# Performance work log

Hardware: AMD Instinct MI355X
Metric: run time of the kernel (lower is better)

The kernel has to match this reference:

```python
import jax, jax.numpy as jnp
import numpy as np

N_OBJ, N_SR, N_V, N_F = 8192, 4096, 4100, 4096
EPS = 1e-8


def setup_inputs() -> dict:
    key = jax.random.key(0)
    k1, k2, k3, k4, k5 = jax.random.split(key, 5)
    obj_points = jax.random.normal(k1, (N_OBJ, 3), jnp.float32)
    sr_points = 0.5 * jax.random.normal(k2, (N_SR, 3), jnp.float32)
    hand_verts = 0.5 * jax.random.normal(k3, (N_V, 3), jnp.float32)
    face_normals = jax.random.normal(k4, (N_F, 3), jnp.float32)
    hand_faces = jax.random.randint(k5, (N_F, 3), 0, N_V)
    return dict(obj_points=obj_points, sr_points=sr_points,
                hand_verts=hand_verts, face_normals=face_normals,
                hand_faces=hand_faces)


def reference(obj_points, sr_points, hand_verts, face_normals, hand_faces):
    # --- get_NN: brute-force nearest hand point for every object point ---
    d2 = (jnp.sum(obj_points**2, -1)[:, None]
          + jnp.sum(sr_points**2, -1)[None, :]
          - 2.0 * obj_points @ sr_points.T)          # [N, M] squared dists
    nn_idx = jnp.argmin(d2, axis=1)                   # [N]
    trg_pts = sr_points[nn_idx]                       # batched_index_select -> [N,3]
    D = trg_pts - obj_points                          # ray directions [N,3]

    # --- ray-triangle intersection (plane test + 3 edge half-plane tests) ---
    # All [F,N,3] intermediates are avoided via triple-product expansion:
    # every quantity reduces to einsums of per-face [F,3] with per-ray [N,3].
    tri = hand_verts[hand_faces]                      # [F,3,3]
    v0, v1, v2 = tri[:, 0], tri[:, 1], tri[:, 2]
    n = face_normals                                  # [F,3]

    denom = jnp.einsum('fk,nk->fn', n, D)             # D . n   [F,N]
    num = jnp.sum(v0 * n, -1)[:, None] - jnp.einsum('fk,nk->fn', n, obj_points)
    dmask = jnp.abs(denom) > EPS
    t = num / jnp.where(dmask, denom, 1.0)            # plane hit parameter [F,N]

    def edge_sign(va, vb):
        # ((vb-va) x (P-va)) . n  with  P = O + t*D, expanded bilinearly
        c = jnp.cross(n, vb - va)                     # [F,3]
        base = (jnp.einsum('fk,nk->fn', c, obj_points)
                - jnp.sum(va * c, -1)[:, None])
        return base + t * jnp.einsum('fk,nk->fn', c, D)

    inside = ((edge_sign(v0, v1) >= 0)
              & (edge_sign(v1, v2) >= 0)
              & (edge_sign(v2, v0) >= 0))
    hit = inside & dmask & (t > EPS)                  # [F,N]

    hit_number = jnp.sum(hit.astype(jnp.int32), axis=0)   # per ray [N]
    interior = (hit_number % 2) != 0                        # odd parity -> inside

    diff = trg_pts - obj_points
    pen_dist = jnp.sqrt(jnp.sum(diff**2 * interior[:, None].astype(diff.dtype)) + 1e-12)

    # --- contact_map_of_m_to_n(obj_points, sr_points) ---
    nn_dist = jnp.sqrt(jnp.maximum(jnp.min(d2, axis=1), 0.0))
    cmap = 1.0 - 2.0 * (jax.nn.sigmoid(100.0 * nn_dist) - 0.5)

    return pen_dist, cmap
```

## Files before the change

### kernel.cpp

```cpp
#include <hip/hip_runtime.h>
#include <math.h>

#define N_OBJ 8192
#define N_SR  4096
#define N_F   4096
#define EPSF  1e-8f
#define EPS2F 1e-16f

typedef float v2f __attribute__((ext_vector_type(2)));
static __device__ __forceinline__ v2f sp(float x) { v2f r; r.x = x; r.y = x; return r; }
static __device__ __forceinline__ v2f vfma(v2f a, v2f b, v2f c) { return __builtin_elementwise_fma(a, b, c); }

__global__ void __launch_bounds__(256) nn_all(const float* __restrict__ obj,
                                              const float* __restrict__ sr,
                                              const float* __restrict__ hv,
                                              const float* __restrict__ fn,
                                              const int* __restrict__ hf,
                                              float* __restrict__ out,
                                              float4* __restrict__ Dws,
                                              float4* __restrict__ F,
                                              int* __restrict__ done) {
    __shared__ float4 pXY[N_SR / 2];
    __shared__ float4 pZS[N_SR / 2];
    const int tid = threadIdx.x, b = blockIdx.x;

    const float2* sr2 = (const float2*)sr;
#pragma unroll
    for (int i = 0; i < 8; ++i) {
        int e = i * 256 + tid;
        float2 A = sr2[3 * e], B = sr2[3 * e + 1], C = sr2[3 * e + 2];
        float x0 = A.x, y0 = A.y, z0 = B.x, x1 = B.y, y1 = C.x, z1 = C.y;
        float s0 = fmaf(x0, x0, fmaf(y0, y0, z0 * z0));
        float s1 = fmaf(x1, x1, fmaf(y1, y1, z1 * z1));
        pXY[e] = make_float4(x0, x1, y0, y1);
        pZS[e] = make_float4(z0, z1, s0, s1);
    }
    if (b == 0 && tid == 0) done[0] = 0;
    if (tid < 8) {
        const int f = b * 8 + tid;
        const int i0 = hf[3*f], i1 = hf[3*f+1], i2 = hf[3*f+2];
        const float v0x = hv[3*i0], v0y = hv[3*i0+1], v0z = hv[3*i0+2];
        const float v1x = hv[3*i1], v1y = hv[3*i1+1], v1z = hv[3*i1+2];
        const float v2x = hv[3*i2], v2y = hv[3*i2+1], v2z = hv[3*i2+2];
        const float nx = fn[3*f], ny = fn[3*f+1], nz = fn[3*f+2];
        F[4*f+0] = make_float4(nx, ny, nz, v0x*nx + v0y*ny + v0z*nz);
        {
            float ex = v1x-v0x, ey = v1y-v0y, ez = v1z-v0z;
            float cx = ny*ez-nz*ey, cy = nz*ex-nx*ez, cz = nx*ey-ny*ex;
            F[4*f+1] = make_float4(cx, cy, cz, v0x*cx + v0y*cy + v0z*cz);
        }
        {
            float ex = v2x-v1x, ey = v2y-v1y, ez = v2z-v1z;
            float cx = ny*ez-nz*ey, cy = nz*ex-nx*ez, cz = nx*ey-ny*ex;
            F[4*f+2] = make_float4(cx, cy, cz, v1x*cx + v1y*cy + v1z*cz);
        }
        {
            float ex = v0x-v2x, ey = v0y-v2y, ez = v0z-v2z;
            float cx = ny*ez-nz*ey, cy = nz*ex-nx*ez, cz = nx*ey-ny*ex;
            F[4*f+3] = make_float4(cx, cy, cz, v2x*cx + v2y*cy + v2z*cz);
        }
    }
    __syncthreads();

    const int w = tid >> 6, lane = tid & 63;
    const int pbase = b * 16 + w * 4;

    float ox[4], oy[4], oz[4], aa[4];
#pragma unroll
    for (int k = 0; k < 4; ++k) {
        int p = pbase + k;
        ox[k] = obj[3*p]; oy[k] = obj[3*p+1]; oz[k] = obj[3*p+2];
        aa[k] = fmaf(ox[k], ox[k], fmaf(oy[k], oy[k], oz[k] * oz[k]));
    }
    float b0[4], b1[4]; int i0[4], i1[4];
#pragma unroll
    for (int k = 0; k < 4; ++k) { b0[k] = b1[k] = INFINITY; i0[k] = 0; i1[k] = 1; }

    int e2 = lane * 2;
#pragma unroll 4
    for (int step = 0; step < 32; ++step) {
        int e = step * 64 + lane;
        float4 A = pXY[e];
        float4 B = pZS[e];
        v2f X; X.x = A.x; X.y = A.y;
        v2f Y; Y.x = A.z; Y.y = A.w;
        v2f Z; Z.x = B.x; Z.y = B.y;
        v2f SS; SS.x = B.z; SS.y = B.w;
#pragma unroll
        for (int k = 0; k < 4; ++k) {
            v2f d  = vfma(Z, sp(oz[k]), vfma(Y, sp(oy[k]), X * sp(ox[k])));
            v2f d2 = vfma(d, sp(-2.f), SS);
            bool c0 = d2.x < b0[k];
            bool c1 = d2.y < b1[k];
            b0[k] = c0 ? d2.x : b0[k];  i0[k] = c0 ? e2     : i0[k];
            b1[k] = c1 ? d2.y : b1[k];  i1[k] = c1 ? e2 + 1 : i1[k];
        }
        e2 += 128;
    }
#pragma unroll
    for (int k = 0; k < 4; ++k) {
        float bd = b0[k]; int bi = i0[k];
        if (b1[k] < bd || (b1[k] == bd && i1[k] < bi)) { bd = b1[k]; bi = i1[k]; }
#pragma unroll
        for (int off = 32; off > 0; off >>= 1) {
            float d = __shfl_down(bd, off);
            int   i = __shfl_down(bi, off);
            if (d < bd || (d == bd && i < bi)) { bd = d; bi = i; }
        }
        if (lane == 0) {
            int p = pbase + k;
            float4 A = pXY[bi >> 1];
            float4 B = pZS[bi >> 1];
            int h = bi & 1;
            float sx = h ? A.y : A.x;
            float sy = h ? A.w : A.z;
            float sz = h ? B.y : B.x;
            float dx = sx - ox[k], dy = sy - oy[k], dz = sz - oz[k];
            Dws[p] = make_float4(dx, dy, dz, fmaf(dx, dx, fmaf(dy, dy, dz * dz)));
            float nn  = sqrtf(fmaxf(bd + aa[k], 0.f));
            float sig = 1.f / (1.f + expf(-100.f * nn));
            out[1 + p] = 1.f - 2.f * (sig - 0.5f);
        }
    }
}

#define RFC 16
__global__ void __launch_bounds__(256) ray_count(const float* __restrict__ obj,
                                                 const float4* __restrict__ Dws,
                                                 const float4* __restrict__ F,
                                                 unsigned char* __restrict__ pcount) {
    __shared__ float4 sF[RFC * 4];
    const int tid = threadIdx.x;
    const int pg = blockIdx.x & 7, fc = blockIdx.x >> 3;

    ((float*)sF)[tid] = ((const float*)(F + (size_t)fc * RFC * 4))[tid];

    float px[4], py[4], pz[4], qx[4], qy[4], qz[4];
    int cnt[4];
#pragma unroll
    for (int h = 0; h < 4; ++h) {
        int p = pg * 1024 + h * 256 + tid;
        px[h] = obj[3*p]; py[h] = obj[3*p+1]; pz[h] = obj[3*p+2];
        float4 D = Dws[p];
        qx[h] = D.x; qy[h] = D.y; qz[h] = D.z;
        cnt[h] = 0;
    }
    __syncthreads();

    float4 nF0 = sF[0], nF1 = sF[1], nF2 = sF[2], nF3 = sF[3];
#pragma unroll 4
    for (int f = 0; f < RFC; ++f) {
        const float4 Fn = nF0, C1 = nF1, C2 = nF2, C3 = nF3;
        if (f + 1 < RFC) {
            nF0 = sF[4*f+4]; nF1 = sF[4*f+5]; nF2 = sF[4*f+6]; nF3 = sF[4*f+7];
        }
#pragma unroll
        for (int h = 0; h < 4; ++h) {
            float denom = fmaf(Fn.z, qz[h], fmaf(Fn.y, qy[h], Fn.x * qx[h]));
            float num   = Fn.w - fmaf(Fn.z, pz[h], fmaf(Fn.y, py[h], Fn.x * px[h]));
            float d2 = denom * denom;
            float nd = num * denom;
            float wx = fmaf(px[h], d2, nd * qx[h]);
            float wy = fmaf(py[h], d2, nd * qy[h]);
            float wz = fmaf(pz[h], d2, nd * qz[h]);
            float q1 = fmaf(-C1.w, d2, fmaf(C1.z, wz, fmaf(C1.y, wy, C1.x * wx)));
            float q2 = fmaf(-C2.w, d2, fmaf(C2.z, wz, fmaf(C2.y, wy, C2.x * wx)));
            float q3 = fmaf(-C3.w, d2, fmaf(C3.z, wz, fmaf(C3.y, wy, C3.x * wx)));
            float tc = fmaf(-EPSF, d2, nd);
            float dc = d2 - EPS2F;
            float m  = fminf(fminf(q1, q2), fminf(q3, fminf(tc, dc)));
            cnt[h] += (m >= 0.f) ? 1 : 0;
        }
    }
#pragma unroll
    for (int h = 0; h < 4; ++h)
        pcount[(size_t)fc * N_OBJ + pg * 1024 + h * 256 + tid] = (unsigned char)cnt[h];
}

#define NCH (N_F / RFC)
__global__ void __launch_bounds__(256) finalize(const float4* __restrict__ Dws,
                                                const unsigned char* __restrict__ pcount,
                                                float* __restrict__ fpart,
                                                int* __restrict__ done,
                                                float* __restrict__ out) {
    __shared__ float wsum[4];
    const int tid = threadIdx.x;
    const int pt = blockIdx.x * 256 + tid;

    int c = 0;
#pragma unroll 8
    for (int fc = 0; fc < NCH; ++fc)
        c += pcount[(size_t)fc * N_OBJ + pt];
    float s = (c & 1) ? Dws[pt].w : 0.f;
#pragma unroll
    for (int off = 32; off > 0; off >>= 1) s += __shfl_down(s, off);
    if ((tid & 63) == 0) wsum[tid >> 6] = s;
    __syncthreads();
    if (tid == 0) {
        fpart[blockIdx.x] = wsum[0] + wsum[1] + wsum[2] + wsum[3];
        __threadfence();
        if (atomicAdd(done, 1) == 31) {
            float tot = 0.f;
            for (int i = 0; i < 32; ++i)
                tot += atomicAdd(&fpart[i], 0.f);
            out[0] = sqrtf(tot + 1e-12f);
        }
    }
}

extern "C" void kernel_launch(void* const* d_in, const int* in_sizes, int n_in,
                              void* d_out, int out_size, void* d_ws, size_t ws_size,
                              hipStream_t stream) {
    const float* obj = (const float*)d_in[0];
    const float* sr  = (const float*)d_in[1];
    const float* hv  = (const float*)d_in[2];
    const float* fn  = (const float*)d_in[3];
    const int*   hf  = (const int*)d_in[4];
    float* out = (float*)d_out;

    char* ws = (char*)d_ws;
    float4*        Dws    = (float4*)(ws + 0);
    float4*        F      = (float4*)(ws + 131072);
    unsigned char* pcount = (unsigned char*)(ws + 393216);
    float*         fpart  = (float*)(ws + 2490368);
    int*           done   = (int*)  (ws + 2490496);

    nn_all<<<512, 256, 0, stream>>>(obj, sr, hv, fn, hf, out, Dws, F, done);
    ray_count<<<2048, 256, 0, stream>>>(obj, Dws, F, pcount);
    finalize<<<32, 256, 0, stream>>>(Dws, pcount, fpart, done, out);
}
```

Before: 116.4 us.

## Chunk NN candidate staging, halve points per block, widen face chunks

The nearest-neighbour kernel now stages the hand points into a small shared chunk (512 pairs) four times instead of the whole 4096-point set. Each block handles 8 object points (2 per wavefront) and the grid doubles to 1024 blocks, which lowers LDS use and raises occupancy but does less ALU work per loaded point. The ray-count kernel processes 64 faces per block over 512 points, so there are 64 face chunks instead of 256. That shrinks the partial-count buffer and the finalize reduction at the cost of fewer registers of ray reuse per thread. Each block now builds the face data for 4 faces.

```diff
diff --git a/kernel.cpp b/kernel.cpp
--- a/kernel.cpp
+++ b/kernel.cpp
@@ -20,24 +20,14 @@
                                               float4* __restrict__ Dws,
                                               float4* __restrict__ F,
                                               int* __restrict__ done) {
-    __shared__ float4 pXY[N_SR / 2];
-    __shared__ float4 pZS[N_SR / 2];
+    __shared__ float4 cXY[512];
+    __shared__ float4 cZS[512];
     const int tid = threadIdx.x, b = blockIdx.x;
-
     const float2* sr2 = (const float2*)sr;
-#pragma unroll
-    for (int i = 0; i < 8; ++i) {
-        int e = i * 256 + tid;
-        float2 A = sr2[3 * e], B = sr2[3 * e + 1], C = sr2[3 * e + 2];
-        float x0 = A.x, y0 = A.y, z0 = B.x, x1 = B.y, y1 = C.x, z1 = C.y;
-        float s0 = fmaf(x0, x0, fmaf(y0, y0, z0 * z0));
-        float s1 = fmaf(x1, x1, fmaf(y1, y1, z1 * z1));
-        pXY[e] = make_float4(x0, x1, y0, y1);
-        pZS[e] = make_float4(z0, z1, s0, s1);
-    }
+
     if (b == 0 && tid == 0) done[0] = 0;
-    if (tid < 8) {
-        const int f = b * 8 + tid;
+    if (tid < 4) {
+        const int f = b * 4 + tid;
         const int i0 = hf[3*f], i1 = hf[3*f+1], i2 = hf[3*f+2];
         const float v0x = hv[3*i0], v0y = hv[3*i0+1], v0z = hv[3*i0+2];
         const float v1x = hv[3*i1], v1y = hv[3*i1+1], v1z = hv[3*i1+2];
@@ -60,86 +50,111 @@
             F[4*f+3] = make_float4(cx, cy, cz, v2x*cx + v2y*cy + v2z*cz);
         }
     }
-    __syncthreads();
 
     const int w = tid >> 6, lane = tid & 63;
-    const int pbase = b * 16 + w * 4;
-
-    float ox[4], oy[4], oz[4], aa[4];
-#pragma unroll
-    for (int k = 0; k < 4; ++k) {
-        int p = pbase + k;
-        ox[k] = obj[3*p]; oy[k] = obj[3*p+1]; oz[k] = obj[3*p+2];
-        aa[k] = fmaf(ox[k], ox[k], fmaf(oy[k], oy[k], oz[k] * oz[k]));
-    }
-    float b0[4], b1[4]; int i0[4], i1[4];
-#pragma unroll
-    for (int k = 0; k < 4; ++k) { b0[k] = b1[k] = INFINITY; i0[k] = 0; i1[k] = 1; }
-
-    int e2 = lane * 2;
-#pragma unroll 4
-    for (int step = 0; step < 32; ++step) {
-        int e = step * 64 + lane;
-        float4 A = pXY[e];
-        float4 B = pZS[e];
-        v2f X; X.x = A.x; X.y = A.y;
-        v2f Y; Y.x = A.z; Y.y = A.w;
-        v2f Z; Z.x = B.x; Z.y = B.y;
-        v2f SS; SS.x = B.z; SS.y = B.w;
-#pragma unroll
-        for (int k = 0; k < 4; ++k) {
-            v2f d  = vfma(Z, sp(oz[k]), vfma(Y, sp(oy[k]), X * sp(ox[k])));
-            v2f d2 = vfma(d, sp(-2.f), SS);
-            bool c0 = d2.x < b0[k];
-            bool c1 = d2.y < b1[k];
-            b0[k] = c0 ? d2.x : b0[k];  i0[k] = c0 ? e2     : i0[k];
-            b1[k] = c1 ? d2.y : b1[k];  i1[k] = c1 ? e2 + 1 : i1[k];
-        }
-        e2 += 128;
-    }
-#pragma unroll
-    for (int k = 0; k < 4; ++k) {
-        float bd = b0[k]; int bi = i0[k];
-        if (b1[k] < bd || (b1[k] == bd && i1[k] < bi)) { bd = b1[k]; bi = i1[k]; }
-#pragma unroll
-        for (int off = 32; off > 0; off >>= 1) {
-            float d = __shfl_down(bd, off);
-            int   i = __shfl_down(bi, off);
-            if (d < bd || (d == bd && i < bi)) { bd = d; bi = i; }
-        }
-        if (lane == 0) {
-            int p = pbase + k;
-            float4 A = pXY[bi >> 1];
-            float4 B = pZS[bi >> 1];
-            int h = bi & 1;
-            float sx = h ? A.y : A.x;
-            float sy = h ? A.w : A.z;
-            float sz = h ? B.y : B.x;
-            float dx = sx - ox[k], dy = sy - oy[k], dz = sz - oz[k];
-            Dws[p] = make_float4(dx, dy, dz, fmaf(dx, dx, fmaf(dy, dy, dz * dz)));
-            float nn  = sqrtf(fmaxf(bd + aa[k], 0.f));
+    const int p0 = b * 8 + w * 2, p1 = p0 + 1;
+
+    const float ax = obj[3*p0], ay = obj[3*p0+1], az = obj[3*p0+2];
+    const float bx = obj[3*p1], by = obj[3*p1+1], bz = obj[3*p1+2];
+    const float aaa = fmaf(ax, ax, fmaf(ay, ay, az * az));
+    const float aab = fmaf(bx, bx, fmaf(by, by, bz * bz));
+
+    float a0 = INFINITY, a1 = INFINITY, c0v = INFINITY, c1v = INFINITY;
+    int ai0 = 0, ai1 = 1, ci0 = 0, ci1 = 1;
+
+    for (int c = 0; c < 4; ++c) {
+        __syncthreads();
+        {
+            int e0 = tid, e1 = tid + 256;
+#pragma unroll
+            for (int t = 0; t < 2; ++t) {
+                int e = t ? e1 : e0;
+                int gp = c * 512 + e;
+                float2 A = sr2[3 * gp], B = sr2[3 * gp + 1], C = sr2[3 * gp + 2];
+                float x0 = A.x, y0 = A.y, z0 = B.x, x1 = B.y, y1 = C.x, z1 = C.y;
+                cXY[e] = make_float4(x0, x1, y0, y1);
+                cZS[e] = make_float4(z0, z1,
+                                     fmaf(x0, x0, fmaf(y0, y0, z0 * z0)),
+                                     fmaf(x1, x1, fmaf(y1, y1, z1 * z1)));
+            }
+        }
+        __syncthreads();
+
+        int e2 = c * 1024 + lane * 2;
+#pragma unroll
+        for (int step = 0; step < 8; ++step) {
+            int e = step * 64 + lane;
+            float4 A = cXY[e];
+            float4 B = cZS[e];
+            v2f X; X.x = A.x; X.y = A.y;
+            v2f Y; Y.x = A.z; Y.y = A.w;
+            v2f Z; Z.x = B.x; Z.y = B.y;
+            v2f SS; SS.x = B.z; SS.y = B.w;
+            {
+                v2f d  = vfma(Z, sp(az), vfma(Y, sp(ay), X * sp(ax)));
+                v2f d2 = vfma(d, sp(-2.f), SS);
+                bool q0 = d2.x < a0, q1 = d2.y < a1;
+                a0 = q0 ? d2.x : a0;  ai0 = q0 ? e2     : ai0;
+                a1 = q1 ? d2.y : a1;  ai1 = q1 ? e2 + 1 : ai1;
+            }
+            {
+                v2f d  = vfma(Z, sp(bz), vfma(Y, sp(by), X * sp(bx)));
+                v2f d2 = vfma(d, sp(-2.f), SS);
+                bool q0 = d2.x < c0v, q1 = d2.y < c1v;
+                c0v = q0 ? d2.x : c0v;  ci0 = q0 ? e2     : ci0;
+                c1v = q1 ? d2.y : c1v;  ci1 = q1 ? e2 + 1 : ci1;
+            }
+            e2 += 128;
+        }
+    }
+
+    float bdA = a0; int biA = ai0;
+    if (a1 < bdA || (a1 == bdA && ai1 < biA)) { bdA = a1; biA = ai1; }
+    float bdB = c0v; int biB = ci0;
+    if (c1v < bdB || (c1v == bdB && ci1 < biB)) { bdB = c1v; biB = ci1; }
+#pragma unroll
+    for (int off = 32; off > 0; off >>= 1) {
+        float d = __shfl_down(bdA, off);
+        int   i = __shfl_down(biA, off);
+        if (d < bdA || (d == bdA && i < biA)) { bdA = d; biA = i; }
+        float e = __shfl_down(bdB, off);
+        int   j = __shfl_down(biB, off);
+        if (e < bdB || (e == bdB && j < biB)) { bdB = e; biB = j; }
+    }
+    if (lane == 0) {
+        {
+            float dx = sr[3*biA] - ax, dy = sr[3*biA+1] - ay, dz = sr[3*biA+2] - az;
+            Dws[p0] = make_float4(dx, dy, dz, fmaf(dx, dx, fmaf(dy, dy, dz * dz)));
+            float nn  = sqrtf(fmaxf(bdA + aaa, 0.f));
             float sig = 1.f / (1.f + expf(-100.f * nn));
-            out[1 + p] = 1.f - 2.f * (sig - 0.5f);
-        }
-    }
-}
-
-#define RFC 16
+            out[1 + p0] = 1.f - 2.f * (sig - 0.5f);
+        }
+        {
+            float dx = sr[3*biB] - bx, dy = sr[3*biB+1] - by, dz = sr[3*biB+2] - bz;
+            Dws[p1] = make_float4(dx, dy, dz, fmaf(dx, dx, fmaf(dy, dy, dz * dz)));
+            float nn  = sqrtf(fmaxf(bdB + aab, 0.f));
+            float sig = 1.f / (1.f + expf(-100.f * nn));
+            out[1 + p1] = 1.f - 2.f * (sig - 0.5f);
+        }
+    }
+}
+
+#define RFC 64
 __global__ void __launch_bounds__(256) ray_count(const float* __restrict__ obj,
                                                  const float4* __restrict__ Dws,
                                                  const float4* __restrict__ F,
                                                  unsigned char* __restrict__ pcount) {
     __shared__ float4 sF[RFC * 4];
     const int tid = threadIdx.x;
-    const int pg = blockIdx.x & 7, fc = blockIdx.x >> 3;
-
-    ((float*)sF)[tid] = ((const float*)(F + (size_t)fc * RFC * 4))[tid];
-
-    float px[4], py[4], pz[4], qx[4], qy[4], qz[4];
-    int cnt[4];
-#pragma unroll
-    for (int h = 0; h < 4; ++h) {
-        int p = pg * 1024 + h * 256 + tid;
+    const int pg = blockIdx.x & 15, fc = blockIdx.x >> 4;
+
+    sF[tid] = (F + (size_t)fc * RFC * 4)[tid];
+
+    float px[2], py[2], pz[2], qx[2], qy[2], qz[2];
+    int cnt[2];
+#pragma unroll
+    for (int h = 0; h < 2; ++h) {
+        int p = pg * 512 + h * 256 + tid;
         px[h] = obj[3*p]; py[h] = obj[3*p+1]; pz[h] = obj[3*p+2];
         float4 D = Dws[p];
         qx[h] = D.x; qy[h] = D.y; qz[h] = D.z;
@@ -155,7 +170,7 @@
             nF0 = sF[4*f+4]; nF1 = sF[4*f+5]; nF2 = sF[4*f+6]; nF3 = sF[4*f+7];
         }
 #pragma unroll
-        for (int h = 0; h < 4; ++h) {
+        for (int h = 0; h < 2; ++h) {
             float denom = fmaf(Fn.z, qz[h], fmaf(Fn.y, qy[h], Fn.x * qx[h]));
             float num   = Fn.w - fmaf(Fn.z, pz[h], fmaf(Fn.y, py[h], Fn.x * px[h]));
             float d2 = denom * denom;
@@ -173,8 +188,8 @@
         }
     }
 #pragma unroll
-    for (int h = 0; h < 4; ++h)
-        pcount[(size_t)fc * N_OBJ + pg * 1024 + h * 256 + tid] = (unsigned char)cnt[h];
+    for (int h = 0; h < 2; ++h)
+        pcount[(size_t)fc * N_OBJ + pg * 512 + h * 256 + tid] = (unsigned char)cnt[h];
 }
 
 #define NCH (N_F / RFC)
@@ -222,10 +237,10 @@
     float4*        Dws    = (float4*)(ws + 0);
     float4*        F      = (float4*)(ws + 131072);
     unsigned char* pcount = (unsigned char*)(ws + 393216);
-    float*         fpart  = (float*)(ws + 2490368);
-    int*           done   = (int*)  (ws + 2490496);
-
-    nn_all<<<512, 256, 0, stream>>>(obj, sr, hv, fn, hf, out, Dws, F, done);
-    ray_count<<<2048, 256, 0, stream>>>(obj, Dws, F, pcount);
+    float*         fpart  = (float*)(ws + 917504);
+    int*           done   = (int*)  (ws + 917632);
+
+    nn_all<<<1024, 256, 0, stream>>>(obj, sr, hv, fn, hf, out, Dws, F, done);
+    ray_count<<<1024, 256, 0, stream>>>(obj, Dws, F, pcount);
     finalize<<<32, 256, 0, stream>>>(Dws, pcount, fpart, done, out);
 }
```

Result: faster. 113.5 us (-2.5%).
